# Kernel tuning notes

Measured on AMD Instinct MI355X. Metric: run time of the kernel, lower is better.

## Reference

```python
import jax, jax.numpy as jnp
import numpy as np

# irreps: node in/out = 32x0e + 16x1o (dim 80), sh = 1x0e + 1x1o (dim 4)
N_NODES, N_EDGES = 8000, 64000
NUM_BASIS, RAD_HIDDEN = 8, 64
WEIGHT_NUMEL = 2304  # 32*32 + 32*16 + 16*16 + 16*32
EPS = 1e-8
INV_SQRT3 = 1.0 / np.sqrt(3.0)
# e3nn path weights (normalization='component', path_normalization='element'):
# into 0e outputs: sqrt(ir.dim=1 / (32+16)); into 1o outputs: sqrt(3 / (32+16))
PW0 = float(np.sqrt(1.0 / 48.0))
PW1 = float(np.sqrt(3.0 / 48.0))


def setup_inputs() -> dict:
    key = jax.random.key(0)
    ks = jax.random.split(key, 10)
    node_features = jax.random.normal(ks[0], (N_NODES, 80), dtype=jnp.float32)
    edge_index = jax.random.randint(ks[1], (2, N_EDGES), 0, N_NODES, dtype=jnp.int64)
    edge_sh = jax.random.normal(ks[2], (N_EDGES, 4), dtype=jnp.float32)
    edge_radial_emb = jax.random.uniform(ks[3], (N_EDGES, NUM_BASIS), dtype=jnp.float32)
    # RadialMLP params (Linear 8->64, SiLU, Linear 64->2304)
    rW1 = jax.random.normal(ks[4], (NUM_BASIS, RAD_HIDDEN), dtype=jnp.float32) / np.sqrt(NUM_BASIS)
    rb1 = jnp.zeros((RAD_HIDDEN,), dtype=jnp.float32)
    rW2 = jax.random.normal(ks[5], (RAD_HIDDEN, WEIGHT_NUMEL), dtype=jnp.float32) / np.sqrt(RAD_HIDDEN)
    rb2 = jnp.zeros((WEIGHT_NUMEL,), dtype=jnp.float32)
    # o3.Linear weights (per-irrep mixing matrices, e3nn init ~ N(0,1))
    Wl0 = jax.random.normal(ks[6], (32, 32), dtype=jnp.float32)
    Wl1 = jax.random.normal(ks[7], (16, 16), dtype=jnp.float32)
    return {"node_features": node_features, "edge_index": edge_index,
            "edge_sh": edge_sh, "edge_radial_emb": edge_radial_emb,
            "rW1": rW1, "rb1": rb1, "rW2": rW2, "rb2": rb2,
            "Wl0": Wl0, "Wl1": Wl1}


def reference(node_features, edge_index, edge_sh, edge_radial_emb,
              rW1, rb1, rW2, rb2, Wl0, Wl1):
    N = node_features.shape[0]
    src, dst = edge_index[0], edge_index[1]
    # radial MLP -> per-edge tensor-product weights [E, 2304] (fp32 path)
    h = jax.nn.silu(edge_radial_emb @ rW1 + rb1)
    tpw = h @ rW2 + rb2
    E = tpw.shape[0]
    wA = tpw[:, :1024].reshape(E, 32, 32)      # 0e x 0e -> 0e
    wB = tpw[:, 1024:1536].reshape(E, 32, 16)  # 0e x 1o -> 1o
    wC = tpw[:, 1536:1792].reshape(E, 16, 16)  # 1o x 0e -> 1o
    wD = tpw[:, 1792:2304].reshape(E, 16, 32)  # 1o x 1o -> 0e
    # gather source node features
    xs = node_features[src, :32]                       # [E,32] scalars
    xv = node_features[src, 32:].reshape(E, 16, 3)     # [E,16,3] vectors
    sh0 = edge_sh[:, 0]                                # [E]
    shv = edge_sh[:, 1:4]                              # [E,3]
    # equivariant tensor product messages
    dotv = jnp.einsum('euk,ek->eu', xv, shv)           # 1o.1o -> 0e
    msg_s = PW0 * (jnp.einsum('euw,eu->ew', wA, xs * sh0[:, None])
                   + INV_SQRT3 * jnp.einsum('euw,eu->eu' if False else 'euw,eu->ew', wD, dotv))
    msg_v = (PW1 * INV_SQRT3) * (jnp.einsum('euw,eu,ek->ewk', wB, xs, shv)
                                 + jnp.einsum('euw,euk->ewk', wC, xv) * sh0[:, None, None])
    messages = jnp.concatenate([msg_s, msg_v.reshape(E, 48)], axis=-1)  # [E,80]
    # scatter-sum aggregation over destination nodes
    agg = jax.ops.segment_sum(messages, dst, num_segments=N)            # [N,80]
    # equivariant linear (per-irrep mixing, fan-in normalized)
    lin_s = (agg[:, :32] @ Wl0) / np.sqrt(32.0)
    lin_v = jnp.einsum('nuk,uv->nvk', agg[:, 32:].reshape(N, 16, 3), Wl1) / np.sqrt(16.0)
    # SafeNormActivation: silu on scalars, norm-gated silu on vectors
    act_s = jax.nn.silu(lin_s)
    norms = jnp.linalg.norm(lin_v, axis=-1, keepdims=True)   # [N,16,1]
    safe = jnp.maximum(norms, EPS)
    act_v = jnp.where(norms < EPS, 0.0, (lin_v / safe) * jax.nn.silu(norms))
    activated = jnp.concatenate([act_s, act_v.reshape(N, 48)], axis=-1)
    # skip connection (irreps_in == irreps_out -> identity skip)
    return node_features + activated
```

## Files before the change

kernel.cpp:

```cpp
#include <hip/hip_runtime.h>
#include <math.h>

#define N_NODES_C 8000
#define N_EDGES_C 64000

static constexpr float PW0_C     = 0.14433756729740646f;
static constexpr float C1_C      = 0.14433756729740643f;
static constexpr float PW0IS3_C  = 0.08333333333333333f;
static constexpr float RS32_C    = 0.17677669529663687f;

typedef __attribute__((ext_vector_type(8))) short short8;
typedef __attribute__((ext_vector_type(4))) float f32x4;

__device__ __forceinline__ float silu_f(float x) { return x / (1.0f + expf(-x)); }

__device__ __forceinline__ unsigned short f2bf(float x) {
    union { float f; unsigned u; } a; a.f = x;
    unsigned r = a.u + 0x7fffu + ((a.u >> 16) & 1u);
    return (unsigned short)(r >> 16);
}

__device__ __forceinline__ void stage16(const void* g, void* lds) {
    __builtin_amdgcn_global_load_lds(
        (const __attribute__((address_space(1))) void*)g,
        (__attribute__((address_space(3))) void*)lds, 16, 0, 0);
}

__global__ __launch_bounds__(256) void prep_kernel(
    const float* __restrict__ rW2, unsigned short* __restrict__ rW2T)
{
    const int idx = blockIdx.x * 256 + threadIdx.x;
    const int k = idx / 2304, col = idx % 2304;
    rW2T[(size_t)col * 64 + k] = f2bf(rW2[idx]);
}

__global__ __launch_bounds__(256, 2) void edge_kernel_mfma(
    const float* __restrict__ nf,
    const int*   __restrict__ ei,
    const float* __restrict__ sh,
    const float* __restrict__ emb,
    const float* __restrict__ rW1,
    const float* __restrict__ rb1,
    const unsigned short* __restrict__ rW2T,
    const float* __restrict__ rb2,
    float* __restrict__ agg)
{
    __shared__ unsigned short hB[64][72];
    __shared__ float xs_s[64][33];
    __shared__ float xv_s[64][52];
    __shared__ float dv_s[64][17];
    __shared__ float sh0_s[64];
    __shared__ float shv_s[64][3];
    __shared__ int   dst_s[64];
    __shared__ float rb2_s[2304];
    __shared__ float pool_f[8192];
    char*  stg = (char*)pool_f;
    float (*msg)[84] = reinterpret_cast<float(*)[84]>(pool_f);

    const int t    = threadIdx.x;
    const int e0   = blockIdx.x * 64;
    const int lane = t & 63, wv = t >> 6;
    const int l15  = lane & 15, lk = lane >> 4;
    const int l7   = l15 & 7;

    #define STAGE(cc, b) {                                                        \
        const char* gsrc = (const char*)rW2T + (size_t)(cc) * 8192;               \
        _Pragma("unroll")                                                         \
        for (int j = 0; j < 2; j++) {                                             \
            const int p  = j * 256 + t;                                           \
            const int pr = p >> 3;                                                \
            const int sl = (p & 7) ^ (pr & 7);                                    \
            stage16(gsrc + pr * 128 + (sl << 4), stg + (b) * 8192 + p * 16);      \
        }                                                                         \
    }

    if (t < 64) {
        const int eid = e0 + t;
        dst_s[t] = ei[N_EDGES_C + eid];
        const float4 s4 = *reinterpret_cast<const float4*>(sh + (size_t)eid * 4);
        sh0_s[t] = s4.x;
        shv_s[t][0] = s4.y; shv_s[t][1] = s4.z; shv_s[t][2] = s4.w;
    }
    STAGE(0, 0)
    STAGE(1, 1)
    {
        const int e = t >> 2, q = t & 3;
        const int src = ei[e0 + e];
        const float* p = nf + (size_t)src * 80 + q * 20;
        #pragma unroll
        for (int f4 = 0; f4 < 5; f4++) {
            const float4 v = *reinterpret_cast<const float4*>(p + f4 * 4);
            const int g = q * 20 + f4 * 4;
            const float vv[4] = {v.x, v.y, v.z, v.w};
            #pragma unroll
            for (int ii = 0; ii < 4; ii++) {
                const int gg = g + ii;
                if (gg < 32) xs_s[e][gg] = vv[ii];
                else         xv_s[e][gg - 32] = vv[ii];
            }
        }
    }
    for (int i = t; i < 2304; i += 256) rb2_s[i] = rb2[i];
    {
        const int c = t & 63, eg = t >> 6;
        float w1[8];
        #pragma unroll
        for (int b = 0; b < 8; b++) w1[b] = rW1[b * 64 + c];
        const float bias = rb1[c];
        #pragma unroll
        for (int rep = 0; rep < 16; rep++) {
            const int e = rep * 4 + eg;
            const float* em = emb + (size_t)(e0 + e) * 8;
            float pre = bias;
            #pragma unroll
            for (int b = 0; b < 8; b++) pre = fmaf(em[b], w1[b], pre);
            hB[e][c] = f2bf(silu_f(pre));
        }
    }
    __syncthreads();
    {
        const int e = t >> 2, q = t & 3;
        #pragma unroll
        for (int i = 0; i < 4; i++) {
            const int u = q * 4 + i;
            dv_s[e][u] = xv_s[e][u*3+0]*shv_s[e][0] + xv_s[e][u*3+1]*shv_s[e][1]
                       + xv_s[e][u*3+2]*shv_s[e][2];
        }
    }
    __syncthreads();

    const int e = wv * 16 + l15;
    const float sh0 = sh0_s[e];
    const float fA  = PW0_C * sh0;
    const short8 bf0 = *reinterpret_cast<const short8*>(&hB[e][lk * 8]);
    const short8 bf1 = *reinterpret_cast<const short8*>(&hB[e][32 + lk * 8]);

    float sA[2][4] = {{0,0,0,0},{0,0,0,0}};
    float sB[4]    = {0,0,0,0};
    float sC[3][4] = {{0,0,0,0},{0,0,0,0},{0,0,0,0}};

    for (int c = 0; c < 36; ++c) {
        if (c < 34) STAGE(c + 2, (c + 2) & 3)
        if (c < 34)       { asm volatile("s_waitcnt vmcnt(4)" ::: "memory"); }
        else if (c == 34) { asm volatile("s_waitcnt vmcnt(2)" ::: "memory"); }
        else              { asm volatile("s_waitcnt vmcnt(0)" ::: "memory"); }
        __builtin_amdgcn_sched_barrier(0);
        __builtin_amdgcn_s_barrier();

        const int cb = c * 64;
        f32x4 acc[4];
        #pragma unroll
        for (int m = 0; m < 4; m++) {
            const float4 rbv = *reinterpret_cast<const float4*>(&rb2_s[cb + m * 16 + lk * 4]);
            acc[m][0] = rbv.x; acc[m][1] = rbv.y; acc[m][2] = rbv.z; acc[m][3] = rbv.w;
        }
        const char* sb = stg + (c & 3) * 8192;
        #pragma unroll
        for (int s = 0; s < 2; s++) {
            const short8 bf = s ? bf1 : bf0;
            #pragma unroll
            for (int m = 0; m < 4; m++) {
                const short8 a = *reinterpret_cast<const short8*>(
                    sb + (m * 16 + l15) * 128 + (((s * 4 + lk) ^ l7) << 4));
                acc[m] = __builtin_amdgcn_mfma_f32_16x16x32_bf16(a, bf, acc[m], 0, 0, 0);
            }
        }

        if (c < 16) {
            const float x0 = xs_s[e][c * 2] * fA, x1 = xs_s[e][c * 2 + 1] * fA;
            #pragma unroll
            for (int r = 0; r < 4; r++) {
                sA[0][r] = fmaf(acc[0][r], x0, fmaf(acc[2][r], x1, sA[0][r]));
                sA[1][r] = fmaf(acc[1][r], x0, fmaf(acc[3][r], x1, sA[1][r]));
            }
        } else if (c < 24) {
            const int u0 = (c - 16) * 4;
            const float x0 = xs_s[e][u0], x1 = xs_s[e][u0+1], x2 = xs_s[e][u0+2], x3 = xs_s[e][u0+3];
            #pragma unroll
            for (int r = 0; r < 4; r++)
                sB[r] = fmaf(acc[0][r], x0, fmaf(acc[1][r], x1,
                         fmaf(acc[2][r], x2, fmaf(acc[3][r], x3, sB[r]))));
        } else if (c < 28) {
            const int u0 = (c - 24) * 4;
            #pragma unroll
            for (int k = 0; k < 3; k++) {
                const float x0 = xv_s[e][(u0+0)*3+k], x1 = xv_s[e][(u0+1)*3+k];
                const float x2 = xv_s[e][(u0+2)*3+k], x3 = xv_s[e][(u0+3)*3+k];
                #pragma unroll
                for (int r = 0; r < 4; r++)
                    sC[k][r] = fmaf(acc[0][r], x0, fmaf(acc[1][r], x1,
                                fmaf(acc[2][r], x2, fmaf(acc[3][r], x3, sC[k][r]))));
            }
        } else {
            const int u0 = (c - 28) * 2;
            const float d0 = dv_s[e][u0] * PW0IS3_C, d1 = dv_s[e][u0 + 1] * PW0IS3_C;
            #pragma unroll
            for (int r = 0; r < 4; r++) {
                sA[0][r] = fmaf(acc[0][r], d0, fmaf(acc[2][r], d1, sA[0][r]));
                sA[1][r] = fmaf(acc[1][r], d0, fmaf(acc[3][r], d1, sA[1][r]));
            }
        }
    }
    #undef STAGE

    #pragma unroll
    for (int hi = 0; hi < 2; hi++)
        #pragma unroll
        for (int r = 0; r < 4; r++)
            msg[e][hi * 16 + lk * 4 + r] = sA[hi][r];
    #pragma unroll
    for (int r = 0; r < 4; r++) {
        const int w = lk * 4 + r;
        #pragma unroll
        for (int k = 0; k < 3; k++)
            msg[e][32 + w * 3 + k] = C1_C * (sB[r] * shv_s[e][k] + sh0 * sC[k][r]);
    }
    __syncthreads();

    for (int i = t; i < 64 * 80; i += 256) {
        const int ee = i / 80, m = i - ee * 80;
        atomicAdd(&agg[(size_t)dst_s[ee] * 80 + m], msg[ee][m]);
    }
}

__global__ __launch_bounds__(256, 1) void edge_kernel_f32(
    const float* __restrict__ nf, const int* __restrict__ ei,
    const float* __restrict__ sh, const float* __restrict__ emb,
    const float* __restrict__ rW1, const float* __restrict__ rb1,
    const float* __restrict__ rW2, const float* __restrict__ rb2,
    float* __restrict__ agg)
{
    __shared__ float hT[64][68];
    __shared__ float tpw[64][132];
    __shared__ float xs_s[64][32];
    __shared__ float xv_s[64][48];
    __shared__ float dv_s[64][16];
    __shared__ float sh0_s[64];
    __shared__ float shv_s[64][3];
    __shared__ int   dst_s[64];
    __shared__ float msg[64][84];

    const int t  = threadIdx.x;
    const int e0 = blockIdx.x * 64;
    if (t < 64) {
        const int eid = e0 + t;
        dst_s[t] = ei[N_EDGES_C + eid];
        const float4 s4 = *reinterpret_cast<const float4*>(sh + (size_t)eid * 4);
        sh0_s[t] = s4.x; shv_s[t][0] = s4.y; shv_s[t][1] = s4.z; shv_s[t][2] = s4.w;
    }
    for (int i = t; i < 64 * 84; i += 256) (&msg[0][0])[i] = 0.0f;
    {
        const int e = t >> 2, q = t & 3;
        const int src = ei[e0 + e];
        const float* p = nf + (size_t)src * 80 + q * 20;
        #pragma unroll
        for (int f4 = 0; f4 < 5; f4++) {
            const float4 v = *reinterpret_cast<const float4*>(p + f4 * 4);
            const int g = q * 20 + f4 * 4;
            const float vv[4] = {v.x, v.y, v.z, v.w};
            #pragma unroll
            for (int ii = 0; ii < 4; ii++) {
                const int gg = g + ii;
                if (gg < 32) xs_s[e][gg] = vv[ii]; else xv_s[e][gg - 32] = vv[ii];
            }
        }
    }
    {
        const int c = t & 63, eg = t >> 6;
        float w1[8];
        #pragma unroll
        for (int b = 0; b < 8; b++) w1[b] = rW1[b * 64 + c];
        const float bias = rb1[c];
        #pragma unroll
        for (int rep = 0; rep < 16; rep++) {
            const int e = rep * 4 + eg;
            const float* em = emb + (size_t)(e0 + e) * 8;
            float pre = bias;
            #pragma unroll
            for (int b = 0; b < 8; b++) pre = fmaf(em[b], w1[b], pre);
            hT[c][e] = silu_f(pre);
        }
    }
    __syncthreads();
    {
        const int e = t >> 2, q = t & 3;
        #pragma unroll
        for (int i = 0; i < 4; i++) {
            const int u = q * 4 + i;
            dv_s[e][u] = xv_s[e][u*3+0]*shv_s[e][0] + xv_s[e][u*3+1]*shv_s[e][1]
                       + xv_s[e][u*3+2]*shv_s[e][2];
        }
    }
    __syncthreads();
    const int lane = t & 63, wv = t >> 6;
    for (int ch = 0; ch < 18; ch++) {
        const int jb = ch * 128;
        float acc[16][2];
        #pragma unroll
        for (int i = 0; i < 16; i++) { acc[i][0] = 0.0f; acc[i][1] = 0.0f; }
        const float* Bp = rW2 + jb + lane * 2;
        #pragma unroll 2
        for (int c = 0; c < 64; c++) {
            const float2 b = *reinterpret_cast<const float2*>(Bp + (size_t)c * 2304);
            const float4* ap = reinterpret_cast<const float4*>(&hT[c][wv * 16]);
            const float4 a0 = ap[0], a1 = ap[1], a2 = ap[2], a3 = ap[3];
            const float va[16] = {a0.x,a0.y,a0.z,a0.w, a1.x,a1.y,a1.z,a1.w,
                                  a2.x,a2.y,a2.z,a2.w, a3.x,a3.y,a3.z,a3.w};
            #pragma unroll
            for (int i = 0; i < 16; i++) {
                acc[i][0] = fmaf(va[i], b.x, acc[i][0]);
                acc[i][1] = fmaf(va[i], b.y, acc[i][1]);
            }
        }
        const float2 rb = *reinterpret_cast<const float2*>(rb2 + jb + lane * 2);
        __syncthreads();
        #pragma unroll
        for (int i = 0; i < 16; i++)
            *reinterpret_cast<float2*>(&tpw[wv * 16 + i][lane * 2]) =
                make_float2(acc[i][0] + rb.x, acc[i][1] + rb.y);
        __syncthreads();
        if (ch < 8) {
            const int u0 = ch * 4, w = t & 31, eg = t >> 5;
            #pragma unroll
            for (int ee = 0; ee < 8; ee++) {
                const int e = eg * 8 + ee;
                float s = 0.0f;
                #pragma unroll
                for (int du = 0; du < 4; du++) s = fmaf(tpw[e][du * 32 + w], xs_s[e][u0 + du], s);
                msg[e][w] = fmaf(PW0_C * sh0_s[e], s, msg[e][w]);
            }
        } else if (ch < 12) {
            const int u0 = (ch - 8) * 8, w = t & 15, eg = t >> 4;
            #pragma unroll
            for (int ee = 0; ee < 4; ee++) {
                const int e = eg * 4 + ee;
                float s = 0.0f;
                #pragma unroll
                for (int du = 0; du < 8; du++) s = fmaf(tpw[e][du * 16 + w], xs_s[e][u0 + du], s);
                const float c1s = C1_C * s;
                msg[e][32 + w*3 + 0] = fmaf(c1s, shv_s[e][0], msg[e][32 + w*3 + 0]);
                msg[e][32 + w*3 + 1] = fmaf(c1s, shv_s[e][1], msg[e][32 + w*3 + 1]);
                msg[e][32 + w*3 + 2] = fmaf(c1s, shv_s[e][2], msg[e][32 + w*3 + 2]);
            }
        } else if (ch < 14) {
            const int u0 = (ch - 12) * 8, w = t & 15, eg = t >> 4;
            #pragma unroll
            for (int ee = 0; ee < 4; ee++) {
                const int e = eg * 4 + ee;
                float s0 = 0, s1 = 0, s2 = 0;
                #pragma unroll
                for (int du = 0; du < 8; du++) {
                    const float tv = tpw[e][du * 16 + w];
                    const int u = u0 + du;
                    s0 = fmaf(tv, xv_s[e][u*3 + 0], s0);
                    s1 = fmaf(tv, xv_s[e][u*3 + 1], s1);
                    s2 = fmaf(tv, xv_s[e][u*3 + 2], s2);
                }
                const float f = C1_C * sh0_s[e];
                msg[e][32 + w*3 + 0] = fmaf(f, s0, msg[e][32 + w*3 + 0]);
                msg[e][32 + w*3 + 1] = fmaf(f, s1, msg[e][32 + w*3 + 1]);
                msg[e][32 + w*3 + 2] = fmaf(f, s2, msg[e][32 + w*3 + 2]);
            }
        } else {
            const int u0 = (ch - 14) * 4, w = t & 31, eg = t >> 5;
            #pragma unroll
            for (int ee = 0; ee < 8; ee++) {
                const int e = eg * 8 + ee;
                float s = 0.0f;
                #pragma unroll
                for (int du = 0; du < 4; du++) s = fmaf(tpw[e][du * 32 + w], dv_s[e][u0 + du], s);
                msg[e][w] = fmaf(PW0IS3_C, s, msg[e][w]);
            }
        }
    }
    __syncthreads();
    for (int i = t; i < 64 * 80; i += 256) {
        const int e = i / 80, m = i - e * 80;
        atomicAdd(&agg[(size_t)dst_s[e] * 80 + m], msg[e][m]);
    }
}

__global__ __launch_bounds__(256, 4) void node_kernel(
    const float* __restrict__ nf,
    float* __restrict__ io,
    const float* __restrict__ Wl0,
    const float* __restrict__ Wl1)
{
    __shared__ float a_s[4][80];
    const int t  = threadIdx.x;
    const int nb = blockIdx.x * 4;
    for (int i = t; i < 320; i += 256)
        a_s[i / 80][i % 80] = io[(size_t)nb * 80 + i];
    __syncthreads();

    const int ln = t >> 6;
    const int r  = t & 63;
    const int n  = nb + ln;
    const float* a = a_s[ln];
    if (r < 32) {
        float s = 0.0f;
        #pragma unroll
        for (int u = 0; u < 32; u++) s = fmaf(a[u], Wl0[u * 32 + r], s);
        s *= RS32_C;
        io[(size_t)n * 80 + r] = nf[(size_t)n * 80 + r] + silu_f(s);
    } else if (r < 48) {
        const int v = r - 32;
        float l0 = 0, l1 = 0, l2 = 0;
        #pragma unroll
        for (int u = 0; u < 16; u++) {
            const float w = Wl1[u * 16 + v];
            l0 = fmaf(a[32 + u*3 + 0], w, l0);
            l1 = fmaf(a[32 + u*3 + 1], w, l1);
            l2 = fmaf(a[32 + u*3 + 2], w, l2);
        }
        l0 *= 0.25f; l1 *= 0.25f; l2 *= 0.25f;
        const float norm = sqrtf(l0*l0 + l1*l1 + l2*l2);
        float f = 0.0f;
        if (norm >= 1e-8f) f = silu_f(norm) / norm;
        const size_t o = (size_t)n * 80 + 32 + (size_t)v * 3;
        io[o + 0] = nf[o + 0] + f * l0;
        io[o + 1] = nf[o + 1] + f * l1;
        io[o + 2] = nf[o + 2] + f * l2;
    }
}

extern "C" void kernel_launch(void* const* d_in, const int* in_sizes, int n_in,
                              void* d_out, int out_size, void* d_ws, size_t ws_size,
                              hipStream_t stream) {
    const float* nf  = (const float*)d_in[0];
    const int*   ei  = (const int*)d_in[1];
    const float* sh  = (const float*)d_in[2];
    const float* emb = (const float*)d_in[3];
    const float* rW1 = (const float*)d_in[4];
    const float* rb1 = (const float*)d_in[5];
    const float* rW2 = (const float*)d_in[6];
    const float* rb2 = (const float*)d_in[7];
    const float* Wl0 = (const float*)d_in[8];
    const float* Wl1 = (const float*)d_in[9];

    float* agg = (float*)d_out;
    hipMemsetAsync(agg, 0, (size_t)N_NODES_C * 80 * sizeof(float), stream);

    const size_t rW2T_bytes = (size_t)2304 * 64 * sizeof(unsigned short);
    if (d_ws != nullptr && ws_size >= rW2T_bytes) {
        unsigned short* rW2T = (unsigned short*)d_ws;
        prep_kernel<<<(2304 * 64) / 256, 256, 0, stream>>>(rW2, rW2T);
        edge_kernel_mfma<<<N_EDGES_C / 64, 256, 0, stream>>>(
            nf, ei, sh, emb, rW1, rb1, rW2T, rb2, agg);
    } else {
        edge_kernel_f32<<<N_EDGES_C / 64, 256, 0, stream>>>(
            nf, ei, sh, emb, rW1, rb1, rW2, rb2, agg);
    }
    node_kernel<<<N_NODES_C / 4, 256, 0, stream>>>(nf, agg, Wl0, Wl1);
}
```

Baseline: 75.24 us.

## Process 128 edges per block to reuse staged rW2 tiles across two edge groups

Each block now handles 128 edges instead of 64, so every staged rW2 chunk in LDS feeds two MFMA streams (two edge sets per wave). This halves the total rW2 staging traffic and the barrier overhead per edge. To fit the larger tile, node features are stored in LDS as bf16, and the radial MLP hidden layer is computed straight into MFMA operand registers with rW1 cached in LDS. The edge grid is halved, which lowers parallelism. Register pressure rises from duplicated accumulators, and bf16 inputs add rounding error.

```diff
diff --git a/kernel.cpp b/kernel.cpp
--- a/kernel.cpp
+++ b/kernel.cpp
@@ -18,6 +18,9 @@
     union { float f; unsigned u; } a; a.f = x;
     unsigned r = a.u + 0x7fffu + ((a.u >> 16) & 1u);
     return (unsigned short)(r >> 16);
+}
+__device__ __forceinline__ float bf2f(unsigned short x) {
+    union { unsigned u; float f; } a; a.u = ((unsigned)x) << 16; return a.f;
 }
 
 __device__ __forceinline__ void stage16(const void* g, void* lds) {
@@ -45,20 +48,21 @@
     const float* __restrict__ rb2,
     float* __restrict__ agg)
 {
-    __shared__ unsigned short hB[64][72];
-    __shared__ float xs_s[64][33];
-    __shared__ float xv_s[64][52];
-    __shared__ float dv_s[64][17];
-    __shared__ float sh0_s[64];
-    __shared__ float shv_s[64][3];
-    __shared__ int   dst_s[64];
+    __shared__ float pool_f[8192];
     __shared__ float rb2_s[2304];
-    __shared__ float pool_f[8192];
+    __shared__ float rW1_s[512];
+    __shared__ unsigned short xs_s[128][34];
+    __shared__ unsigned short xv_s[128][50];
+    __shared__ float dv_s[128][17];
+    __shared__ float sh0_s[128];
+    __shared__ float shv_s[128][3];
+    __shared__ int   dst_s[128];
+
     char*  stg = (char*)pool_f;
     float (*msg)[84] = reinterpret_cast<float(*)[84]>(pool_f);
 
     const int t    = threadIdx.x;
-    const int e0   = blockIdx.x * 64;
+    const int e0   = blockIdx.x * 128;
     const int lane = t & 63, wv = t >> 6;
     const int l15  = lane & 15, lk = lane >> 4;
     const int l7   = l15 & 7;
@@ -74,70 +78,98 @@
         }                                                                         \
     }
 
-    if (t < 64) {
+    STAGE(0, 0)
+    STAGE(1, 1)
+    if (t < 128) {
         const int eid = e0 + t;
         dst_s[t] = ei[N_EDGES_C + eid];
         const float4 s4 = *reinterpret_cast<const float4*>(sh + (size_t)eid * 4);
         sh0_s[t] = s4.x;
         shv_s[t][0] = s4.y; shv_s[t][1] = s4.z; shv_s[t][2] = s4.w;
     }
-    STAGE(0, 0)
-    STAGE(1, 1)
     {
-        const int e = t >> 2, q = t & 3;
+        const int e = t >> 1, q = t & 1;
         const int src = ei[e0 + e];
-        const float* p = nf + (size_t)src * 80 + q * 20;
-        #pragma unroll
-        for (int f4 = 0; f4 < 5; f4++) {
+        const float* p = nf + (size_t)src * 80 + q * 40;
+        #pragma unroll
+        for (int f4 = 0; f4 < 10; f4++) {
             const float4 v = *reinterpret_cast<const float4*>(p + f4 * 4);
-            const int g = q * 20 + f4 * 4;
+            const int g = q * 40 + f4 * 4;
             const float vv[4] = {v.x, v.y, v.z, v.w};
             #pragma unroll
             for (int ii = 0; ii < 4; ii++) {
                 const int gg = g + ii;
-                if (gg < 32) xs_s[e][gg] = vv[ii];
-                else         xv_s[e][gg - 32] = vv[ii];
-            }
-        }
-    }
+                if (gg < 32) xs_s[e][gg]      = f2bf(vv[ii]);
+                else         xv_s[e][gg - 32] = f2bf(vv[ii]);
+            }
+        }
+    }
+    for (int i = t; i < 512;  i += 256) rW1_s[i] = rW1[i];
     for (int i = t; i < 2304; i += 256) rb2_s[i] = rb2[i];
+    __syncthreads();
+
     {
-        const int c = t & 63, eg = t >> 6;
-        float w1[8];
-        #pragma unroll
-        for (int b = 0; b < 8; b++) w1[b] = rW1[b * 64 + c];
-        const float bias = rb1[c];
-        #pragma unroll
-        for (int rep = 0; rep < 16; rep++) {
-            const int e = rep * 4 + eg;
-            const float* em = emb + (size_t)(e0 + e) * 8;
-            float pre = bias;
-            #pragma unroll
-            for (int b = 0; b < 8; b++) pre = fmaf(em[b], w1[b], pre);
-            hB[e][c] = f2bf(silu_f(pre));
-        }
-    }
+        const int e = t >> 1, u0d = (t & 1) * 8;
+        #pragma unroll
+        for (int i = 0; i < 8; i++) {
+            const int u = u0d + i;
+            dv_s[e][u] = bf2f(xv_s[e][u*3+0]) * shv_s[e][0]
+                       + bf2f(xv_s[e][u*3+1]) * shv_s[e][1]
+                       + bf2f(xv_s[e][u*3+2]) * shv_s[e][2];
+        }
+    }
+    const int eA = wv * 32 + l15;
+    const int eB = eA + 16;
+    short8 bfr[2][2];
+    {
+        float embA[8], embB[8];
+        {
+            const float* pa = emb + (size_t)(e0 + eA) * 8;
+            const float* pb = emb + (size_t)(e0 + eB) * 8;
+            const float4 a0 = *reinterpret_cast<const float4*>(pa);
+            const float4 a1 = *reinterpret_cast<const float4*>(pa + 4);
+            const float4 b0 = *reinterpret_cast<const float4*>(pb);
+            const float4 b1 = *reinterpret_cast<const float4*>(pb + 4);
+            embA[0]=a0.x; embA[1]=a0.y; embA[2]=a0.z; embA[3]=a0.w;
+            embA[4]=a1.x; embA[5]=a1.y; embA[6]=a1.z; embA[7]=a1.w;
+            embB[0]=b0.x; embB[1]=b0.y; embB[2]=b0.z; embB[3]=b0.w;
+            embB[4]=b1.x; embB[5]=b1.y; embB[6]=b1.z; embB[7]=b1.w;
+        }
+        #pragma unroll
+        for (int s = 0; s < 2; s++) {
+            const int k0 = s * 32 + lk * 8;
+            const float4 r0 = *reinterpret_cast<const float4*>(rb1 + k0);
+            const float4 r1 = *reinterpret_cast<const float4*>(rb1 + k0 + 4);
+            float preA[8] = {r0.x,r0.y,r0.z,r0.w, r1.x,r1.y,r1.z,r1.w};
+            float preB[8] = {r0.x,r0.y,r0.z,r0.w, r1.x,r1.y,r1.z,r1.w};
+            #pragma unroll
+            for (int b = 0; b < 8; b++) {
+                const float4 wa = *reinterpret_cast<const float4*>(&rW1_s[b * 64 + k0]);
+                const float4 wb = *reinterpret_cast<const float4*>(&rW1_s[b * 64 + k0 + 4]);
+                const float wv4[8] = {wa.x,wa.y,wa.z,wa.w, wb.x,wb.y,wb.z,wb.w};
+                #pragma unroll
+                for (int j = 0; j < 8; j++) {
+                    preA[j] = fmaf(embA[b], wv4[j], preA[j]);
+                    preB[j] = fmaf(embB[b], wv4[j], preB[j]);
+                }
+            }
+            short8 hA, hBv;
+            #pragma unroll
+            for (int j = 0; j < 8; j++) {
+                hA[j]  = (short)f2bf(silu_f(preA[j]));
+                hBv[j] = (short)f2bf(silu_f(preB[j]));
+            }
+            bfr[0][s] = hA; bfr[1][s] = hBv;
+        }
+    }
+    const float sh0A = sh0_s[eA], sh0B = sh0_s[eB];
+    const float fAA  = PW0_C * sh0A, fAB = PW0_C * sh0B;
     __syncthreads();
-    {
-        const int e = t >> 2, q = t & 3;
-        #pragma unroll
-        for (int i = 0; i < 4; i++) {
-            const int u = q * 4 + i;
-            dv_s[e][u] = xv_s[e][u*3+0]*shv_s[e][0] + xv_s[e][u*3+1]*shv_s[e][1]
-                       + xv_s[e][u*3+2]*shv_s[e][2];
-        }
-    }
-    __syncthreads();
-
-    const int e = wv * 16 + l15;
-    const float sh0 = sh0_s[e];
-    const float fA  = PW0_C * sh0;
-    const short8 bf0 = *reinterpret_cast<const short8*>(&hB[e][lk * 8]);
-    const short8 bf1 = *reinterpret_cast<const short8*>(&hB[e][32 + lk * 8]);
-
-    float sA[2][4] = {{0,0,0,0},{0,0,0,0}};
-    float sB[4]    = {0,0,0,0};
-    float sC[3][4] = {{0,0,0,0},{0,0,0,0},{0,0,0,0}};
+
+    float sA0[2][4] = {{0,0,0,0},{0,0,0,0}}, sA1[2][4] = {{0,0,0,0},{0,0,0,0}};
+    float sB0[4] = {0,0,0,0},                sB1[4] = {0,0,0,0};
+    float sC0[3][4] = {{0,0,0,0},{0,0,0,0},{0,0,0,0}};
+    float sC1[3][4] = {{0,0,0,0},{0,0,0,0},{0,0,0,0}};
 
     for (int c = 0; c < 36; ++c) {
         if (c < 34) STAGE(c + 2, (c + 2) & 3)
@@ -148,78 +180,109 @@
         __builtin_amdgcn_s_barrier();
 
         const int cb = c * 64;
-        f32x4 acc[4];
+        f32x4 acc0[4], acc1[4];
         #pragma unroll
         for (int m = 0; m < 4; m++) {
             const float4 rbv = *reinterpret_cast<const float4*>(&rb2_s[cb + m * 16 + lk * 4]);
-            acc[m][0] = rbv.x; acc[m][1] = rbv.y; acc[m][2] = rbv.z; acc[m][3] = rbv.w;
+            acc0[m][0] = rbv.x; acc0[m][1] = rbv.y; acc0[m][2] = rbv.z; acc0[m][3] = rbv.w;
+            acc1[m][0] = rbv.x; acc1[m][1] = rbv.y; acc1[m][2] = rbv.z; acc1[m][3] = rbv.w;
         }
         const char* sb = stg + (c & 3) * 8192;
         #pragma unroll
         for (int s = 0; s < 2; s++) {
-            const short8 bf = s ? bf1 : bf0;
             #pragma unroll
             for (int m = 0; m < 4; m++) {
                 const short8 a = *reinterpret_cast<const short8*>(
                     sb + (m * 16 + l15) * 128 + (((s * 4 + lk) ^ l7) << 4));
-                acc[m] = __builtin_amdgcn_mfma_f32_16x16x32_bf16(a, bf, acc[m], 0, 0, 0);
+                acc0[m] = __builtin_amdgcn_mfma_f32_16x16x32_bf16(a, bfr[0][s], acc0[m], 0, 0, 0);
+                acc1[m] = __builtin_amdgcn_mfma_f32_16x16x32_bf16(a, bfr[1][s], acc1[m], 0, 0, 0);
             }
         }
 
         if (c < 16) {
-            const float x0 = xs_s[e][c * 2] * fA, x1 = xs_s[e][c * 2 + 1] * fA;
+            const float xA0 = bf2f(xs_s[eA][c*2]) * fAA, xA1 = bf2f(xs_s[eA][c*2+1]) * fAA;
+            const float xB0 = bf2f(xs_s[eB][c*2]) * fAB, xB1 = bf2f(xs_s[eB][c*2+1]) * fAB;
             #pragma unroll
             for (int r = 0; r < 4; r++) {
-                sA[0][r] = fmaf(acc[0][r], x0, fmaf(acc[2][r], x1, sA[0][r]));
-                sA[1][r] = fmaf(acc[1][r], x0, fmaf(acc[3][r], x1, sA[1][r]));
+                sA0[0][r] = fmaf(acc0[0][r], xA0, fmaf(acc0[2][r], xA1, sA0[0][r]));
+                sA0[1][r] = fmaf(acc0[1][r], xA0, fmaf(acc0[3][r], xA1, sA0[1][r]));
+                sA1[0][r] = fmaf(acc1[0][r], xB0, fmaf(acc1[2][r], xB1, sA1[0][r]));
+                sA1[1][r] = fmaf(acc1[1][r], xB0, fmaf(acc1[3][r], xB1, sA1[1][r]));
             }
         } else if (c < 24) {
             const int u0 = (c - 16) * 4;
-            const float x0 = xs_s[e][u0], x1 = xs_s[e][u0+1], x2 = xs_s[e][u0+2], x3 = xs_s[e][u0+3];
-            #pragma unroll
-            for (int r = 0; r < 4; r++)
-                sB[r] = fmaf(acc[0][r], x0, fmaf(acc[1][r], x1,
-                         fmaf(acc[2][r], x2, fmaf(acc[3][r], x3, sB[r]))));
+            float xA[4], xB[4];
+            #pragma unroll
+            for (int m = 0; m < 4; m++) { xA[m] = bf2f(xs_s[eA][u0+m]); xB[m] = bf2f(xs_s[eB][u0+m]); }
+            #pragma unroll
+            for (int r = 0; r < 4; r++) {
+                sB0[r] = fmaf(acc0[0][r], xA[0], fmaf(acc0[1][r], xA[1],
+                          fmaf(acc0[2][r], xA[2], fmaf(acc0[3][r], xA[3], sB0[r]))));
+                sB1[r] = fmaf(acc1[0][r], xB[0], fmaf(acc1[1][r], xB[1],
+                          fmaf(acc1[2][r], xB[2], fmaf(acc1[3][r], xB[3], sB1[r]))));
+            }
         } else if (c < 28) {
             const int u0 = (c - 24) * 4;
             #pragma unroll
             for (int k = 0; k < 3; k++) {
-                const float x0 = xv_s[e][(u0+0)*3+k], x1 = xv_s[e][(u0+1)*3+k];
-                const float x2 = xv_s[e][(u0+2)*3+k], x3 = xv_s[e][(u0+3)*3+k];
-                #pragma unroll
-                for (int r = 0; r < 4; r++)
-                    sC[k][r] = fmaf(acc[0][r], x0, fmaf(acc[1][r], x1,
-                                fmaf(acc[2][r], x2, fmaf(acc[3][r], x3, sC[k][r]))));
+                float xA[4], xB[4];
+                #pragma unroll
+                for (int m = 0; m < 4; m++) {
+                    xA[m] = bf2f(xv_s[eA][(u0+m)*3+k]);
+                    xB[m] = bf2f(xv_s[eB][(u0+m)*3+k]);
+                }
+                #pragma unroll
+                for (int r = 0; r < 4; r++) {
+                    sC0[k][r] = fmaf(acc0[0][r], xA[0], fmaf(acc0[1][r], xA[1],
+                                 fmaf(acc0[2][r], xA[2], fmaf(acc0[3][r], xA[3], sC0[k][r]))));
+                    sC1[k][r] = fmaf(acc1[0][r], xB[0], fmaf(acc1[1][r], xB[1],
+                                 fmaf(acc1[2][r], xB[2], fmaf(acc1[3][r], xB[3], sC1[k][r]))));
+                }
             }
         } else {
             const int u0 = (c - 28) * 2;
-            const float d0 = dv_s[e][u0] * PW0IS3_C, d1 = dv_s[e][u0 + 1] * PW0IS3_C;
+            const float dA0 = dv_s[eA][u0] * PW0IS3_C, dA1 = dv_s[eA][u0+1] * PW0IS3_C;
+            const float dB0 = dv_s[eB][u0] * PW0IS3_C, dB1 = dv_s[eB][u0+1] * PW0IS3_C;
             #pragma unroll
             for (int r = 0; r < 4; r++) {
-                sA[0][r] = fmaf(acc[0][r], d0, fmaf(acc[2][r], d1, sA[0][r]));
-                sA[1][r] = fmaf(acc[1][r], d0, fmaf(acc[3][r], d1, sA[1][r]));
+                sA0[0][r] = fmaf(acc0[0][r], dA0, fmaf(acc0[2][r], dA1, sA0[0][r]));
+                sA0[1][r] = fmaf(acc0[1][r], dA0, fmaf(acc0[3][r], dA1, sA0[1][r]));
+                sA1[0][r] = fmaf(acc1[0][r], dB0, fmaf(acc1[2][r], dB1, sA1[0][r]));
+                sA1[1][r] = fmaf(acc1[1][r], dB0, fmaf(acc1[3][r], dB1, sA1[1][r]));
             }
         }
     }
     #undef STAGE
 
     #pragma unroll
-    for (int hi = 0; hi < 2; hi++)
-        #pragma unroll
-        for (int r = 0; r < 4; r++)
-            msg[e][hi * 16 + lk * 4 + r] = sA[hi][r];
-    #pragma unroll
-    for (int r = 0; r < 4; r++) {
-        const int w = lk * 4 + r;
-        #pragma unroll
-        for (int k = 0; k < 3; k++)
-            msg[e][32 + w * 3 + k] = C1_C * (sB[r] * shv_s[e][k] + sh0 * sC[k][r]);
-    }
-    __syncthreads();
-
-    for (int i = t; i < 64 * 80; i += 256) {
-        const int ee = i / 80, m = i - ee * 80;
-        atomicAdd(&agg[(size_t)dst_s[ee] * 80 + m], msg[ee][m]);
+    for (int pass = 0; pass < 2; ++pass) {
+        __syncthreads();
+        if ((wv >> 1) == pass) {
+            const int lr0 = (wv & 1) * 32 + l15;
+            const int lr1 = lr0 + 16;
+            #pragma unroll
+            for (int hi = 0; hi < 2; hi++)
+                #pragma unroll
+                for (int r = 0; r < 4; r++) {
+                    msg[lr0][hi * 16 + lk * 4 + r] = sA0[hi][r];
+                    msg[lr1][hi * 16 + lk * 4 + r] = sA1[hi][r];
+                }
+            #pragma unroll
+            for (int r = 0; r < 4; r++) {
+                const int w = lk * 4 + r;
+                #pragma unroll
+                for (int k = 0; k < 3; k++) {
+                    msg[lr0][32 + w * 3 + k] = C1_C * (sB0[r] * shv_s[eA][k] + sh0A * sC0[k][r]);
+                    msg[lr1][32 + w * 3 + k] = C1_C * (sB1[r] * shv_s[eB][k] + sh0B * sC1[k][r]);
+                }
+            }
+        }
+        __syncthreads();
+        const int ebase = pass * 64;
+        for (int i = t; i < 64 * 80; i += 256) {
+            const int rr = i / 80, m = i - rr * 80;
+            atomicAdd(&agg[(size_t)dst_s[ebase + rr] * 80 + m], msg[rr][m]);
+        }
     }
 }
 
@@ -445,7 +508,7 @@
     if (d_ws != nullptr && ws_size >= rW2T_bytes) {
         unsigned short* rW2T = (unsigned short*)d_ws;
         prep_kernel<<<(2304 * 64) / 256, 256, 0, stream>>>(rW2, rW2T);
-        edge_kernel_mfma<<<N_EDGES_C / 64, 256, 0, stream>>>(
+        edge_kernel_mfma<<<N_EDGES_C / 128, 256, 0, stream>>>(
             nf, ei, sh, emb, rW1, rb1, rW2T, rb2, agg);
     } else {
         edge_kernel_f32<<<N_EDGES_C / 64, 256, 0, stream>>>(
```

Result: faster. 69.63 us (-7.5%).
